# Kernel optimization log

Measured on AMD Instinct MI355X. Metric: run time of the kernel, lower is better.

The kernel has to match this reference:

```python
import jax, jax.numpy as jnp
import numpy as np

D_MODEL = 256
N_HEAD = 4
HEAD_DIM = D_MODEL // N_HEAD  # 64


def setup_inputs() -> dict:
    key = jax.random.key(0)
    kx, kw, kb = jax.random.split(key, 3)
    x = jax.random.normal(kx, (4, 2048, D_MODEL), dtype=jnp.float32)
    # nn.Linear(256, 768): weight [768, 256], bias [768]
    bound = 1.0 / np.sqrt(D_MODEL)
    W_qkv = jax.random.uniform(kw, (3 * D_MODEL, D_MODEL), dtype=jnp.float32, minval=-bound, maxval=bound)
    b_qkv = jax.random.uniform(kb, (3 * D_MODEL,), dtype=jnp.float32, minval=-bound, maxval=bound)
    return {"x": x, "W_qkv": W_qkv, "b_qkv": b_qkv}


def reference(x, W_qkv, b_qkv):
    B, S, _ = x.shape
    # fused QKV projection: [B, S, 3*D]
    qkv = jnp.einsum("bsd,ed->bse", x, W_qkv) + b_qkv
    q, k, v = jnp.split(qkv, 3, axis=-1)
    # [B, S, D] -> [B, H, S, Dh]
    def to_heads(t):
        return t.reshape(B, S, N_HEAD, HEAD_DIM).transpose(0, 2, 1, 3)
    q, k, v = to_heads(q), to_heads(k), to_heads(v)
    scale = 1.0 / np.sqrt(HEAD_DIM)
    # scores [B, H, S, S]
    scores = jnp.einsum("bhqd,bhkd->bhqk", q, k) * scale
    attn = jax.nn.softmax(scores, axis=-1)
    out = jnp.einsum("bhqk,bhkd->bhqd", attn, v)  # [B, H, S, Dh]
    return out
```

## Files before the change

### kernel.cpp

```cpp
#include <hip/hip_runtime.h>

#define BB 4
#define SS 2048
#define DM 256
#define NH 4
#define DH 64
#define NROW (BB*SS)
#define NE   (3*DM)
#define BH   (BB*NH)
#define HEAD_ELEMS (BH*SS*DH)
#define NQROWS (BH*SS)
#define NKZ 4

typedef _Float16 half_t;
typedef __attribute__((ext_vector_type(8))) _Float16 half8;
typedef __attribute__((ext_vector_type(4))) _Float16 half4;
typedef __attribute__((ext_vector_type(4))) float floatx4;

#define KPAD 72

#define QK_SCALE 0.18033688011112042f
#define EXP2(x) __builtin_amdgcn_exp2f(x)
#define DEFER_THR 8.0f

__global__ __launch_bounds__(256) void prep(const float* __restrict__ W,
                                            half_t* __restrict__ wh) {
    int gtid = blockIdx.x * 256 + threadIdx.x;
    int i = gtid * 4;
    float4 v = *(const float4*)&W[i];
    half4 h;
    h.x = (half_t)v.x; h.y = (half_t)v.y;
    h.z = (half_t)v.z; h.w = (half_t)v.w;
    *(half4*)&wh[i] = h;
}

__global__ __launch_bounds__(256) void qkv_proj(const float* __restrict__ x,
                                                const half_t* __restrict__ whg,
                                                const float* __restrict__ bias,
                                                half_t* __restrict__ qh,
                                                half_t* __restrict__ kh,
                                                half_t* __restrict__ vt) {
    __shared__ __align__(16) half_t Xh[64 * KPAD];
    __shared__ __align__(16) half_t Wh[64 * KPAD];

    const int rb   = blockIdx.x * 64;
    const int nb   = blockIdx.y * 64;
    const int tid  = threadIdx.x;
    const int wid  = tid >> 6;
    const int lane = tid & 63;
    const int quad = lane >> 4;
    const int col  = lane & 15;

    floatx4 acc[4];
    #pragma unroll
    for (int t = 0; t < 4; ++t) acc[t] = (floatx4){0.f, 0.f, 0.f, 0.f};

    for (int k0 = 0; k0 < DM; k0 += 64) {
        __syncthreads();
        #pragma unroll
        for (int i = 0; i < 2; ++i) {
            int gi = tid + 256 * i;
            int r  = gi >> 3;
            int c8 = (gi & 7) * 8;
            const float* xp = &x[(size_t)(rb + r) * DM + k0 + c8];
            float4 v0 = *(const float4*)xp;
            float4 v1 = *(const float4*)(xp + 4);
            half8 h;
            h[0] = (half_t)v0.x; h[1] = (half_t)v0.y;
            h[2] = (half_t)v0.z; h[3] = (half_t)v0.w;
            h[4] = (half_t)v1.x; h[5] = (half_t)v1.y;
            h[6] = (half_t)v1.z; h[7] = (half_t)v1.w;
            *(half8*)&Xh[r * KPAD + c8] = h;
            *(half8*)&Wh[r * KPAD + c8] = *(const half8*)&whg[(size_t)(nb + r) * DM + k0 + c8];
        }
        __syncthreads();

        half8 ah0 = *(const half8*)&Xh[(wid * 16 + col) * KPAD + quad * 8];
        half8 ah1 = *(const half8*)&Xh[(wid * 16 + col) * KPAD + 32 + quad * 8];

        #pragma unroll
        for (int t = 0; t < 4; ++t) {
            half8 bh0 = *(const half8*)&Wh[(t * 16 + col) * KPAD + quad * 8];
            half8 bh1 = *(const half8*)&Wh[(t * 16 + col) * KPAD + 32 + quad * 8];
            acc[t] = __builtin_amdgcn_mfma_f32_16x16x32_f16(ah0, bh0, acc[t], 0, 0, 0);
            acc[t] = __builtin_amdgcn_mfma_f32_16x16x32_f16(ah1, bh1, acc[t], 0, 0, 0);
        }
    }

    const int part = nb >> 8;
    const int mloc = wid * 16 + quad * 4;
    if (part != 2) {
        #pragma unroll
        for (int t = 0; t < 4; ++t) {
            int e    = nb + t * 16 + col;
            float be = bias[e];
            int dm   = e & 255;
            int h    = dm >> 6;
            int dh   = dm & 63;
            #pragma unroll
            for (int r = 0; r < 4; ++r) {
                int row = rb + mloc + r;
                int b   = row >> 11;
                int s   = row & 2047;
                int bh_ = b * NH + h;
                float val = acc[t][r] + be;
                if (part == 0) {
                    qh[((size_t)bh_ * SS + s) * DH + dh] = (half_t)(val * QK_SCALE);
                } else {
                    kh[((size_t)bh_ * SS + s) * DH + dh] = (half_t)val;
                }
            }
        }
    } else {
        __syncthreads();
        #pragma unroll
        for (int t = 0; t < 4; ++t) {
            int e    = nb + t * 16 + col;
            float be = bias[e];
            #pragma unroll
            for (int r = 0; r < 4; ++r)
                Xh[(t * 16 + col) * KPAD + mloc + r] = (half_t)(acc[t][r] + be);
        }
        __syncthreads();
        const int b   = rb >> 11;
        const int s0  = rb & 2047;
        const int h   = (nb >> 6) & 3;
        const int bh_ = b * NH + h;
        #pragma unroll
        for (int i = 0; i < 2; ++i) {
            int idx = tid + 256 * i;
            int rr  = idx >> 3;
            int cc8 = (idx & 7) * 8;
            *(half8*)&vt[((size_t)bh_ * DH + rr) * SS + s0 + cc8] =
                *(const half8*)&Xh[rr * KPAD + cc8];
        }
    }
}

__global__ __launch_bounds__(256) void attn(const half_t* __restrict__ qh,
                                            const half_t* __restrict__ kh,
                                            const half_t* __restrict__ vt,
                                            half_t* __restrict__ pO,
                                            float* __restrict__ mst,
                                            float* __restrict__ lst) {
    __shared__ __align__(16) half_t Ks[64 * KPAD];
    __shared__ __align__(16) half_t Vts[64 * KPAD];

    const int lin  = blockIdx.x + 16 * blockIdx.y + 256 * blockIdx.z;
    const int xcd  = lin & 7;
    const int j    = lin >> 3;
    const int strm = xcd + 8 * (j >> 4);
    const int q0   = (j & 15) * 128;
    const int bh   = strm & 15;
    const int kz   = strm >> 4;

    const size_t base = (size_t)bh * SS * DH;
    const int tid  = threadIdx.x;
    const int wid  = tid >> 6;
    const int lane = tid & 63;
    const int quad = lane >> 4;
    const int col  = lane & 15;
    const int ktBeg = kz * (SS / NKZ);
    const int ktEnd = ktBeg + (SS / NKZ);

    int srr[2], scc[2];
    #pragma unroll
    for (int i = 0; i < 2; ++i) {
        int gi = tid + 256 * i;
        srr[i] = gi >> 3;
        scc[i] = (gi & 7) * 8;
    }

    half8 bq[2][2];
    #pragma unroll
    for (int st = 0; st < 2; ++st) {
        int s = q0 + wid * 32 + st * 16 + col;
        bq[st][0] = *(const half8*)&qh[base + (size_t)s * DH + quad * 8];
        bq[st][1] = *(const half8*)&qh[base + (size_t)s * DH + 32 + quad * 8];
    }

    half8 nk[2], nv[2];
    #pragma unroll
    for (int i = 0; i < 2; ++i) {
        nk[i] = *(const half8*)&kh[base + (size_t)(ktBeg + srr[i]) * DH + scc[i]];
        nv[i] = *(const half8*)&vt[base + (size_t)srr[i] * SS + ktBeg + scc[i]];
    }

    float m_i[2]    = {-3.0e38f, -3.0e38f};
    float l_part[2] = {0.f, 0.f};
    floatx4 o[2][4];
    #pragma unroll
    for (int st = 0; st < 2; ++st)
        #pragma unroll
        for (int dt = 0; dt < 4; ++dt) o[st][dt] = (floatx4){0.f, 0.f, 0.f, 0.f};

    for (int kt = ktBeg; kt < ktEnd; kt += 64) {
        __syncthreads();
        #pragma unroll
        for (int i = 0; i < 2; ++i) {
            *(half8*)&Ks[srr[i] * KPAD + scc[i]]  = nk[i];
            *(half8*)&Vts[srr[i] * KPAD + scc[i]] = nv[i];
        }
        __syncthreads();

        const int ktn = kt + 64;
        if (ktn < ktEnd) {
            #pragma unroll
            for (int i = 0; i < 2; ++i) {
                nk[i] = *(const half8*)&kh[base + (size_t)(ktn + srr[i]) * DH + scc[i]];
                nv[i] = *(const half8*)&vt[base + (size_t)srr[i] * SS + ktn + scc[i]];
            }
        }

        floatx4 sc[2][4];
        #pragma unroll
        for (int t = 0; t < 4; ++t) {
            half8 ak0 = *(const half8*)&Ks[(t * 16 + col) * KPAD + quad * 8];
            half8 ak1 = *(const half8*)&Ks[(t * 16 + col) * KPAD + 32 + quad * 8];
            #pragma unroll
            for (int st = 0; st < 2; ++st) {
                floatx4 c = (floatx4){0.f, 0.f, 0.f, 0.f};
                c = __builtin_amdgcn_mfma_f32_16x16x32_f16(ak0, bq[st][0], c, 0, 0, 0);
                c = __builtin_amdgcn_mfma_f32_16x16x32_f16(ak1, bq[st][1], c, 0, 0, 0);
                sc[st][t] = c;
            }
        }

        half4 pa[2][4];
        #pragma unroll
        for (int st = 0; st < 2; ++st) {
            float mloc = -3.0e38f;
            #pragma unroll
            for (int t = 0; t < 4; ++t) {
                float a = fmaxf(fmaxf(sc[st][t][0], sc[st][t][1]),
                                fmaxf(sc[st][t][2], sc[st][t][3]));
                mloc = fmaxf(mloc, a);
            }
            mloc = fmaxf(mloc, __shfl_xor(mloc, 16));
            mloc = fmaxf(mloc, __shfl_xor(mloc, 32));

            bool skip = __all(mloc <= m_i[st] + DEFER_THR);
            float m_new = skip ? m_i[st] : fmaxf(m_i[st], mloc);

            float rsumL = 0.f;
            #pragma unroll
            for (int t = 0; t < 4; ++t) {
                float p0 = EXP2(sc[st][t][0] - m_new);
                float p1 = EXP2(sc[st][t][1] - m_new);
                float p2 = EXP2(sc[st][t][2] - m_new);
                float p3 = EXP2(sc[st][t][3] - m_new);
                rsumL += p0 + p1 + p2 + p3;
                pa[st][t] = (half4){(half_t)p0, (half_t)p1, (half_t)p2, (half_t)p3};
            }

            if (skip) {
                l_part[st] += rsumL;
            } else {
                float alpha = EXP2(m_i[st] - m_new);
                m_i[st] = m_new;
                l_part[st] = l_part[st] * alpha + rsumL;
                float ar[4];
                #pragma unroll
                for (int i = 0; i < 4; ++i) ar[i] = __shfl(alpha, quad * 4 + i);
                #pragma unroll
                for (int dt = 0; dt < 4; ++dt)
                    #pragma unroll
                    for (int i = 0; i < 4; ++i)
                        o[st][dt][i] *= ar[i];
            }
        }

        #pragma unroll
        for (int t = 0; t < 4; ++t) {
            #pragma unroll
            for (int dt = 0; dt < 4; ++dt) {
                half4 bv = *(const half4*)&Vts[(dt * 16 + col) * KPAD + t * 16 + quad * 4];
                #pragma unroll
                for (int st = 0; st < 2; ++st)
                    o[st][dt] = __builtin_amdgcn_mfma_f32_16x16x16f16(pa[st][t], bv, o[st][dt], 0, 0, 0);
            }
        }
    }

    const size_t pbase = (size_t)kz * HEAD_ELEMS + base;
    #pragma unroll
    for (int st = 0; st < 2; ++st) {
        float l_i = l_part[st] + __shfl_xor(l_part[st], 16);
        l_i += __shfl_xor(l_i, 32);
        float inv = 1.0f / l_i;
        float ir[4];
        #pragma unroll
        for (int i = 0; i < 4; ++i) ir[i] = __shfl(inv, quad * 4 + i);
        #pragma unroll
        for (int dt = 0; dt < 4; ++dt)
            #pragma unroll
            for (int i = 0; i < 4; ++i) {
                int row = q0 + wid * 32 + st * 16 + quad * 4 + i;
                pO[pbase + (size_t)row * DH + dt * 16 + col] = (half_t)(o[st][dt][i] * ir[i]);
            }
        if (quad == 0) {
            int row = q0 + wid * 32 + st * 16 + col;
            int idx = kz * NQROWS + bh * SS + row;
            mst[idx] = m_i[st];
            lst[idx] = l_i;
        }
    }
}

__global__ __launch_bounds__(256) void merge(const half_t* __restrict__ pO,
                                             const float* __restrict__ mst,
                                             const float* __restrict__ lst,
                                             float* __restrict__ out) {
    int gid = blockIdx.x * 256 + threadIdx.x;
    int row = gid >> 3;
    int dc  = (gid & 7) * 8;
    float m[NKZ], l[NKZ];
    #pragma unroll
    for (int p = 0; p < NKZ; ++p) {
        m[p] = mst[p * NQROWS + row];
        l[p] = lst[p * NQROWS + row];
    }
    float M = fmaxf(fmaxf(m[0], m[1]), fmaxf(m[2], m[3]));
    float w[NKZ], wsum = 0.f;
    #pragma unroll
    for (int p = 0; p < NKZ; ++p) { w[p] = l[p] * EXP2(m[p] - M); wsum += w[p]; }
    float inv = 1.0f / wsum;

    float r[8] = {0.f,0.f,0.f,0.f,0.f,0.f,0.f,0.f};
    #pragma unroll
    for (int p = 0; p < NKZ; ++p) {
        float a = w[p] * inv;
        half8 ov = *(const half8*)&pO[(size_t)p * HEAD_ELEMS + (size_t)row * DH + dc];
        #pragma unroll
        for (int e = 0; e < 8; ++e) r[e] += a * (float)ov[e];
    }
    float4 r0 = {r[0], r[1], r[2], r[3]};
    float4 r1 = {r[4], r[5], r[6], r[7]};
    *(float4*)&out[(size_t)row * DH + dc]     = r0;
    *(float4*)&out[(size_t)row * DH + dc + 4] = r1;
}

extern "C" void kernel_launch(void* const* d_in, const int* in_sizes, int n_in,
                              void* d_out, int out_size, void* d_ws, size_t ws_size,
                              hipStream_t stream) {
    const float* x  = (const float*)d_in[0];
    const float* Wq = (const float*)d_in[1];
    const float* bq = (const float*)d_in[2];
    float* out = (float*)d_out;

    half_t* qh  = (half_t*)d_ws;
    half_t* kh  = qh + (size_t)HEAD_ELEMS;
    half_t* vt  = kh + (size_t)HEAD_ELEMS;
    half_t* whp = (half_t*)d_ws + (size_t)5 * HEAD_ELEMS;
    half_t* pO  = (half_t*)d_ws + (size_t)6 * HEAD_ELEMS;
    float*  mst = (float*)((char*)d_ws + (size_t)10 * HEAD_ELEMS * 2);
    float*  lst = mst + (size_t)NKZ * NQROWS;

    prep<<<192, 256, 0, stream>>>(Wq, whp);
    qkv_proj<<<dim3(NROW / 64, NE / 64), 256, 0, stream>>>(x, whp, bq, qh, kh, vt);
    attn<<<dim3(SS / 128, BH, NKZ), 256, 0, stream>>>(qh, kh, vt, pO, mst, lst);
    merge<<<1024, 256, 0, stream>>>(pO, mst, lst, out);
}
```

Baseline: 112.0 us.

## Fuse split-K merge into attention via last-block atomic counter

Drops the separate merge kernel. Each attention block bumps a per-(head, query-tile) atomic counter, and the last of the four split-K blocks to finish does the log-sum-exp merge of the partial outputs and writes the final result. The prep kernel zeroes the counters. This removes one kernel launch and lets the merge overlap with other attention blocks, at the cost of threadfences, an atomic per block, and a serial merge tail in whichever block finishes last.

```diff
diff --git a/kernel.cpp b/kernel.cpp
--- a/kernel.cpp
+++ b/kernel.cpp
@@ -24,7 +24,9 @@
 #define DEFER_THR 8.0f
 
 __global__ __launch_bounds__(256) void prep(const float* __restrict__ W,
-                                            half_t* __restrict__ wh) {
+                                            half_t* __restrict__ wh,
+                                            int* __restrict__ cnt) {
+    if (blockIdx.x == 0) cnt[threadIdx.x] = 0;
     int gtid = blockIdx.x * 256 + threadIdx.x;
     int i = gtid * 4;
     float4 v = *(const float4*)&W[i];
@@ -142,7 +144,9 @@
                                             const half_t* __restrict__ vt,
                                             half_t* __restrict__ pO,
                                             float* __restrict__ mst,
-                                            float* __restrict__ lst) {
+                                            float* __restrict__ lst,
+                                            int* __restrict__ cnt,
+                                            float* __restrict__ out) {
     __shared__ __align__(16) half_t Ks[64 * KPAD];
     __shared__ __align__(16) half_t Vts[64 * KPAD];
 
@@ -305,39 +309,47 @@
             lst[idx] = l_i;
         }
     }
-}
-
-__global__ __launch_bounds__(256) void merge(const half_t* __restrict__ pO,
-                                             const float* __restrict__ mst,
-                                             const float* __restrict__ lst,
-                                             float* __restrict__ out) {
-    int gid = blockIdx.x * 256 + threadIdx.x;
-    int row = gid >> 3;
-    int dc  = (gid & 7) * 8;
-    float m[NKZ], l[NKZ];
-    #pragma unroll
-    for (int p = 0; p < NKZ; ++p) {
-        m[p] = mst[p * NQROWS + row];
-        l[p] = lst[p * NQROWS + row];
-    }
-    float M = fmaxf(fmaxf(m[0], m[1]), fmaxf(m[2], m[3]));
-    float w[NKZ], wsum = 0.f;
-    #pragma unroll
-    for (int p = 0; p < NKZ; ++p) { w[p] = l[p] * EXP2(m[p] - M); wsum += w[p]; }
-    float inv = 1.0f / wsum;
-
-    float r[8] = {0.f,0.f,0.f,0.f,0.f,0.f,0.f,0.f};
-    #pragma unroll
-    for (int p = 0; p < NKZ; ++p) {
-        float a = w[p] * inv;
-        half8 ov = *(const half8*)&pO[(size_t)p * HEAD_ELEMS + (size_t)row * DH + dc];
-        #pragma unroll
-        for (int e = 0; e < 8; ++e) r[e] += a * (float)ov[e];
-    }
-    float4 r0 = {r[0], r[1], r[2], r[3]};
-    float4 r1 = {r[4], r[5], r[6], r[7]};
-    *(float4*)&out[(size_t)row * DH + dc]     = r0;
-    *(float4*)&out[(size_t)row * DH + dc + 4] = r1;
+
+    __shared__ int lastf;
+    __threadfence();
+    __syncthreads();
+    if (tid == 0)
+        lastf = ((atomicAdd(cnt + (bh * 16 + (j & 15)), 1) & 3) == 3);
+    __syncthreads();
+    if (lastf) {
+        __threadfence();
+        #pragma unroll
+        for (int it = 0; it < 4; ++it) {
+            int idx = tid + 256 * it;
+            int rl  = idx >> 3;
+            int dc  = (idx & 7) * 8;
+            int row = bh * SS + q0 + rl;
+            float m[NKZ], l[NKZ];
+            #pragma unroll
+            for (int p = 0; p < NKZ; ++p) {
+                m[p] = mst[p * NQROWS + row];
+                l[p] = lst[p * NQROWS + row];
+            }
+            float M = fmaxf(fmaxf(m[0], m[1]), fmaxf(m[2], m[3]));
+            float w[NKZ], wsum = 0.f;
+            #pragma unroll
+            for (int p = 0; p < NKZ; ++p) { w[p] = l[p] * EXP2(m[p] - M); wsum += w[p]; }
+            float inv2 = 1.0f / wsum;
+
+            float r[8] = {0.f,0.f,0.f,0.f,0.f,0.f,0.f,0.f};
+            #pragma unroll
+            for (int p = 0; p < NKZ; ++p) {
+                float a = w[p] * inv2;
+                half8 ov = *(const half8*)&pO[(size_t)p * HEAD_ELEMS + (size_t)row * DH + dc];
+                #pragma unroll
+                for (int e = 0; e < 8; ++e) r[e] += a * (float)ov[e];
+            }
+            float4 r0 = {r[0], r[1], r[2], r[3]};
+            float4 r1 = {r[4], r[5], r[6], r[7]};
+            *(float4*)&out[(size_t)row * DH + dc]     = r0;
+            *(float4*)&out[(size_t)row * DH + dc + 4] = r1;
+        }
+    }
 }
 
 extern "C" void kernel_launch(void* const* d_in, const int* in_sizes, int n_in,
@@ -355,9 +367,9 @@
     half_t* pO  = (half_t*)d_ws + (size_t)6 * HEAD_ELEMS;
     float*  mst = (float*)((char*)d_ws + (size_t)10 * HEAD_ELEMS * 2);
     float*  lst = mst + (size_t)NKZ * NQROWS;
-
-    prep<<<192, 256, 0, stream>>>(Wq, whp);
+    int*    cnt = (int*)(lst + (size_t)NKZ * NQROWS);
+
+    prep<<<192, 256, 0, stream>>>(Wq, whp, cnt);
     qkv_proj<<<dim3(NROW / 64, NE / 64), 256, 0, stream>>>(x, whp, bq, qh, kh, vt);
-    attn<<<dim3(SS / 128, BH, NKZ), 256, 0, stream>>>(qh, kh, vt, pO, mst, lst);
-    merge<<<1024, 256, 0, stream>>>(pO, mst, lst, out);
+    attn<<<dim3(SS / 128, BH, NKZ), 256, 0, stream>>>(qh, kh, vt, pO, mst, lst, cnt, out);
 }
```

Result: slower. 271.4 us (+142.3%).
